# Kernel tuning notes

Measured on AMD Instinct MI355X. Metric: run time of the kernel, lower is better.

The kernel has to match this reference:

```python
import jax, jax.numpy as jnp
import numpy as np

SENS = 200
DM = 128
NMAPS = 2
NLAYERS = 2
TH = 0.01
EPS = 1e-5
BATCH = 8
SEQ = 96
HEADS = 8


def setup_inputs() -> dict:
    key = jax.random.key(0)
    ks = jax.random.split(key, 8)
    x = jax.random.normal(ks[0], (BATCH, SENS, SEQ, DM), jnp.float32)
    attn_s = jax.random.uniform(ks[1], (1, BATCH, HEADS, SENS, SENS), jnp.float32)
    supports = jax.random.uniform(ks[2], (SENS, SENS), jnp.float32)
    W_conv = jax.random.normal(ks[3], (NMAPS, NLAYERS, DM, DM), jnp.float32) * 0.05
    b_conv = jnp.zeros((NMAPS, NLAYERS, DM), jnp.float32)
    bn_gamma = jnp.ones((NMAPS, DM), jnp.float32)
    bn_beta = jnp.zeros((NMAPS, DM), jnp.float32)
    W_out = jax.random.normal(ks[4], (NMAPS * DM, DM), jnp.float32) * 0.05
    b_out = jnp.zeros((DM,), jnp.float32)
    return dict(x=x, attn_s=attn_s, supports=supports, W_conv=W_conv,
                b_conv=b_conv, bn_gamma=bn_gamma, bn_beta=bn_beta,
                W_out=W_out, b_out=b_out)


def _process_map(A):
    # make_symmetric: lower triangle + mirrored strict lower triangle
    A = jnp.tril(A) + jnp.tril(A, -1).T
    # clamp: threshold on absolute value; note original returns |A| thresholded
    Aa = jnp.abs(A)
    A = jnp.where(Aa > TH, Aa, jnp.zeros_like(Aa))
    # SparseTensor.from_dense(A).t()
    return A.T


def _gcn_norm(adj_t):
    # GCNConv default: add self-loops (weight 1), symmetric D^-1/2 A D^-1/2
    A = adj_t + jnp.eye(adj_t.shape[0], dtype=adj_t.dtype)
    deg = A.sum(axis=1)
    d = jnp.where(deg > 0, jax.lax.rsqrt(deg), jnp.zeros_like(deg))
    return d[:, None] * A * d[None, :]


def reference(x, attn_s, supports, W_conv, b_conv, bn_gamma, bn_beta, W_out, b_out):
    B, N, S, D = x.shape
    # reshape_mat: [B,N,S,D] -> [B*S, N, D]
    xr = x.transpose(0, 2, 1, 3).reshape(B * S, N, D)

    # supports: [data map, adaptive map from attention (mean over batch, heads)]
    maps = [_process_map(supports), _process_map(attn_s[0].mean(axis=(0, 1)))]

    gcn_outputs = []
    for i in range(NMAPS):
        An = _gcn_norm(maps[i])  # [N,N]
        h = jnp.zeros_like(xr[..., :1]) * 0.0  # placeholder replaced below
        h = None
        for l in range(NLAYERS):
            xw = jnp.einsum('bnf,fg->bng', xr, W_conv[i, l])
            hl = jnp.einsum('mn,bng->bmg', An, xw) + b_conv[i, l]
            h = hl if h is None else h + hl
        # BatchNorm1d over feature channel (training-mode batch stats, biased var)
        mu = h.mean(axis=(0, 1))
        var = h.var(axis=(0, 1))
        hn = (h - mu) * jax.lax.rsqrt(var + EPS) * bn_gamma[i] + bn_beta[i]
        gcn_outputs.append(jax.nn.relu(hn))

    cat = jnp.concatenate(gcn_outputs, axis=-1)  # [B*S, N, NMAPS*DM]
    y = jax.nn.relu(jnp.einsum('bnc,cd->bnd', cat, W_out) + b_out)
    # inverse_reshape_mat: [B*S, N, D] -> [B, N, S, D]
    return y.reshape(B, S, N, D).transpose(0, 2, 1, 3)
```

## Files before the change

kernel.cpp:

```cpp
#include <hip/hip_runtime.h>

#define SENS 200
#define DM 128
#define SEQ 96
#define NB 8
#define BS 768
#define NTOT 153600
#define TH 0.01f
#define BN_EPS 1e-5f
#define MPAD 224
#define KP 208
#define ASROW 68

typedef __attribute__((ext_vector_type(8)))  __bf16 bf16x8;
typedef __attribute__((ext_vector_type(4)))  __bf16 bf16x4;
typedef __attribute__((ext_vector_type(16))) float  f32x16;

__device__ __forceinline__ f32x16 mfma32(bf16x8 a, bf16x8 b, f32x16 c) {
    return __builtin_amdgcn_mfma_f32_32x32x16_bf16(a, b, c, 0, 0, 0);
}
__device__ __forceinline__ bf16x8 join8(bf16x4 a, bf16x4 b) {
    bf16x8 r;
    #pragma unroll
    for (int j = 0; j < 4; ++j) { r[j] = a[j]; r[j + 4] = b[j]; }
    return r;
}

__global__ void attn_mean_kernel(const float* __restrict__ attn, float* __restrict__ mapA) {
    int idx = blockIdx.x * 256 + threadIdx.x;
    if (idx >= SENS * SENS) return;
    float s = 0.f;
    #pragma unroll 8
    for (int q = 0; q < 64; ++q) s += attn[(size_t)q * SENS * SENS + idx];
    mapA[idx] = s * (1.0f / 64.0f);
}

__global__ void build_map_kernel(const float* __restrict__ supports, const float* __restrict__ mapA,
                                 float* __restrict__ M, float* __restrict__ deg) {
    __shared__ float red[256];
    int m = blockIdx.x, map = blockIdx.y, j = threadIdx.x;
    const float* src = (map == 0) ? supports : mapA;
    float v = 0.f;
    if (j < SENS) {
        float sym = (m >= j) ? src[m * SENS + j] : src[j * SENS + m];
        float a = fabsf(sym);
        v = (a > TH) ? a : 0.f;
        M[(size_t)map * SENS * SENS + m * SENS + j] = v;
    }
    red[j] = v;
    __syncthreads();
    for (int off = 128; off > 0; off >>= 1) {
        if (j < off) red[j] += red[j + off];
        __syncthreads();
    }
    if (j == 0) deg[map * SENS + m] = red[0] + 1.0f;
}

__global__ __launch_bounds__(256) void prep2_kernel(
    const float* __restrict__ M, const float* __restrict__ deg,
    const float* __restrict__ W_conv, const float* __restrict__ b_conv,
    const float* __restrict__ W_out,
    __bf16* __restrict__ Anb, __bf16* __restrict__ Wt, __bf16* __restrict__ Wot,
    float* __restrict__ bsum, float* __restrict__ bnacc)
{
    const int bid = blockIdx.x, t = threadIdx.x;
    if (bid < 2 * MPAD) {
        const int map = bid / MPAD, m = bid % MPAD;
        const int j = t;
        if (j < KP) {
            float val = 0.f;
            if (m < SENS && j < SENS) {
                float a = M[((size_t)map * SENS + m) * SENS + j] + ((m == j) ? 1.f : 0.f);
                val = rsqrtf(deg[map * SENS + m]) * a * rsqrtf(deg[map * SENS + j]);
            }
            Anb[(((size_t)map * 13 + (j >> 4)) * MPAD + m) * 16 + (j & 15)] = (__bf16)val;
        }
    } else {
        const int idx = (bid - 2 * MPAD) * 256 + t;
        if (idx < 32768) {
            const int map = idx >> 14, g = (idx >> 7) & 127, f = idx & 127;
            const float* wp = W_conv + (size_t)map * 2 * DM * DM + f * DM + g;
            Wt[(((size_t)map * 8 + (f >> 4)) * DM + g) * 16 + (f & 15)] = (__bf16)(wp[0] + wp[DM * DM]);
        } else if (idx < 65536) {
            const int k = idx - 32768, d = k >> 8, c = k & 255;
            Wot[(((size_t)(c >> 4)) * DM + d) * 16 + (c & 15)] = (__bf16)W_out[c * DM + d];
        } else if (idx < 65792) {
            const int k = idx - 65536, map = k >> 7, g = k & 127;
            bsum[k] = b_conv[(map * 2) * DM + g] + b_conv[(map * 2 + 1) * DM + g];
        } else if (idx < 66304) {
            bnacc[idx - 65792] = 0.f;
        }
    }
}

__global__ __launch_bounds__(256) void xprep_kernel(const float* __restrict__ x,
                                                    __bf16* __restrict__ xk) {
    const int n = blockIdx.x, b = blockIdx.y, t = threadIdx.x;
    const float* xp = x + ((size_t)b * SENS + n) * SEQ * DM;
    #pragma unroll 4
    for (int it = 0; it < 12; ++it) {
        const int idx = it * 1024 + t * 4;
        const int s = idx >> 7, f = idx & 127;
        float4 v = make_float4(0.f, 0.f, 0.f, 0.f);
        if (n < SENS) v = *(const float4*)(xp + idx);
        bf16x4 o;
        o[0] = (__bf16)v.x; o[1] = (__bf16)v.y; o[2] = (__bf16)v.z; o[3] = (__bf16)v.w;
        *(bf16x4*)(xk + (((size_t)(b * SEQ + s) * 8 + (f >> 4)) * MPAD + n) * 16 + (f & 15)) = o;
    }
}

__global__ __launch_bounds__(448, 6) void conv_kernel(
    const __bf16* __restrict__ xk, const __bf16* __restrict__ Anb,
    const __bf16* __restrict__ Wt, const float* __restrict__ bsum,
    __bf16* __restrict__ h, float* __restrict__ bnacc)
{
    __shared__ __bf16 xw[64 * KP];
    const int bx = blockIdx.x;
    const int bs = bx >> 2, map = (bx >> 1) & 1, gh = bx & 1;
    const int t = threadIdx.x, w = t >> 6, lane = t & 63;
    const int l31 = lane & 31, hi = lane >> 5;

    {
        f32x16 acc[2];
        #pragma unroll
        for (int p = 0; p < 2; ++p)
            #pragma unroll
            for (int r = 0; r < 16; ++r) acc[p][r] = 0.f;
        const __bf16* xb = xk + (((size_t)bs * 8) * MPAD + w * 32 + l31) * 16 + hi * 8;
        const __bf16* wb = Wt + (((size_t)map * 8) * DM + gh * 64 + l31) * 16 + hi * 8;
        #pragma unroll
        for (int kh = 0; kh < 2; ++kh) {
            bf16x8 bfr[4];
            #pragma unroll
            for (int q = 0; q < 4; ++q)
                bfr[q] = *(const bf16x8*)(xb + (size_t)(kh * 4 + q) * MPAD * 16);
            #pragma unroll
            for (int q = 0; q < 4; ++q) {
                const __bf16* wp = wb + (size_t)(kh * 4 + q) * DM * 16;
                acc[0] = mfma32(*(const bf16x8*)wp, bfr[q], acc[0]);
                acc[1] = mfma32(*(const bf16x8*)(wp + 32 * 16), bfr[q], acc[1]);
            }
        }
        const int n = w * 32 + l31;
        if (n < KP) {
            #pragma unroll
            for (int p = 0; p < 2; ++p)
                #pragma unroll
                for (int r = 0; r < 16; ++r) {
                    const int g = p * 32 + (r & 3) + 8 * (r >> 2) + 4 * hi;
                    xw[g * KP + n] = (__bf16)acc[p][r];
                }
        }
    }
    __syncthreads();

    f32x16 acc2[2];
    #pragma unroll
    for (int p = 0; p < 2; ++p)
        #pragma unroll
        for (int r = 0; r < 16; ++r) acc2[p][r] = 0.f;
    {
        const __bf16* ab = Anb + (((size_t)map * 13) * MPAD + w * 32 + l31) * 16 + hi * 8;
        #pragma unroll
        for (int kc = 0; kc < 13; ++kc) {
            bf16x8 afrag = *(const bf16x8*)(ab + (size_t)kc * MPAD * 16);
            #pragma unroll
            for (int p = 0; p < 2; ++p) {
                bf16x8 bfrag = *(const bf16x8*)(xw + (p * 32 + l31) * KP + kc * 16 + hi * 8);
                acc2[p] = mfma32(afrag, bfrag, acc2[p]);
            }
        }
    }
    float bsn[2], bsq[2];
    #pragma unroll
    for (int p = 0; p < 2; ++p) {
        const float bias = bsum[map * DM + gh * 64 + p * 32 + l31];
        bf16x8 h0, h1;
        float s = 0.f, q = 0.f;
        #pragma unroll
        for (int r = 0; r < 16; ++r) {
            const float v = acc2[p][r] + bias;
            if (r < 8) h0[r] = (__bf16)v; else h1[r - 8] = (__bf16)v;
            const int m = w * 32 + (r & 3) + 8 * (r >> 2) + 4 * hi;
            if (m < SENS) { s += v; q += v * v; }
        }
        __bf16* hp = h + ((((size_t)(bs * 2 + map) * 7 + w) * 4 + (gh * 2 + p)) * 64 + lane) * 16;
        *(bf16x8*)hp = h0;
        *(bf16x8*)(hp + 8) = h1;
        s += __shfl_xor(s, 32);
        q += __shfl_xor(q, 32);
        bsn[p] = s; bsq[p] = q;
    }
    __syncthreads();
    float* red = (float*)xw;
    if (hi == 0) {
        #pragma unroll
        for (int p = 0; p < 2; ++p) {
            red[(p * 32 + l31) * 7 + w] = bsn[p];
            red[(64 + p * 32 + l31) * 7 + w] = bsq[p];
        }
    }
    __syncthreads();
    if (t < 128) {
        const int sq = t >> 6, g = t & 63;
        float s = 0.f;
        #pragma unroll
        for (int k = 0; k < 7; ++k) s += red[(sq * 64 + g) * 7 + k];
        atomicAdd(&bnacc[sq * 256 + map * DM + gh * 64 + g], s);
    }
}

__device__ __forceinline__ void out_stage(int cn, int t, int bs,
                                          const __bf16* __restrict__ h,
                                          const float* sc_s, const float* sh_s,
                                          __bf16* dst)
{
    const int mapn = cn >> 1;
    const __bf16* hb = h + ((size_t)(bs * 2 + mapn) * 28 + (cn & 1) * 2) * 1024;
    bf16x8 vv[4];
    #pragma unroll
    for (int it = 0; it < 4; ++it) {
        const int idx = it * 512 + t;
        if (idx < 1792)
            vv[it] = *(const bf16x8*)(hb + ((size_t)(idx >> 8) * 4 + ((idx >> 7) & 1)) * 1024
                                          + ((idx >> 1) & 63) * 16 + (idx & 1) * 8);
    }
    #pragma unroll
    for (int it = 0; it < 4; ++it) {
        const int idx = it * 512 + t;
        if (idx < 1792) {
            const int half = idx & 1, lane_s = (idx >> 1) & 63;
            const int ctl = (idx >> 7) & 1, strip = idx >> 8;
            const int cl = ctl * 32 + (lane_s & 31);
            const int cg = mapn * DM + (cn & 1) * 64 + cl;
            const float scv = sc_s[cg], shv = sh_s[cg];
            const int mbase = strip * 32 + 4 * (lane_s >> 5) + 16 * half;
            #pragma unroll
            for (int q2 = 0; q2 < 8; ++q2) {
                const int row = mbase + (q2 & 3) + 8 * (q2 >> 2);
                const float fv = (float)vv[it][q2] * scv + shv;
                dst[row * ASROW + cl] = (__bf16)fmaxf(fv, 0.f);
            }
        }
    }
}

__global__ __launch_bounds__(512) void out_kernel(
    const __bf16* __restrict__ h, const __bf16* __restrict__ Wot,
    const float* __restrict__ bnacc,
    const float* __restrict__ gamma, const float* __restrict__ beta,
    const float* __restrict__ b_out, float* __restrict__ out)
{
    __shared__ __bf16 As[2][MPAD * ASROW];
    __shared__ float sc_s[256], sh_s[256];
    const int bs = blockIdx.x;
    const int b = bs / SEQ, s = bs % SEQ;
    const int t = threadIdx.x, w = t >> 6, lane = t & 63;
    const int l31 = lane & 31, hi = lane >> 5;
    const int dct = w & 3, sbase = w >> 2;
    if (t < 256) {
        const float mu = bnacc[t] * (1.f / (float)NTOT);
        const float var = bnacc[256 + t] * (1.f / (float)NTOT) - mu * mu;
        const float sc = gamma[t] * rsqrtf(var + BN_EPS);
        sc_s[t] = sc;
        sh_s[t] = beta[t] - mu * sc;
    }
    f32x16 acc[4];
    {
        const float bo = b_out[dct * 32 + l31];
        #pragma unroll
        for (int i = 0; i < 4; ++i)
            #pragma unroll
            for (int r = 0; r < 16; ++r) acc[i][r] = bo;
    }
    __syncthreads();
    out_stage(0, t, bs, h, sc_s, sh_s, &As[0][0]);
    __syncthreads();
    for (int c = 0; c < 4; ++c) {
        #pragma unroll
        for (int kc = 0; kc < 4; ++kc) {
            bf16x8 bfrag = *(const bf16x8*)(Wot + ((size_t)(c * 4 + kc) * DM + dct * 32 + l31) * 16 + hi * 8);
            #pragma unroll
            for (int i = 0; i < 4; ++i) {
                const int strip = sbase + 2 * i;
                if (strip >= 7) break;
                const __bf16* ap = &As[c & 1][(strip * 32 + l31) * ASROW + kc * 16 + hi * 8];
                acc[i] = mfma32(join8(*(const bf16x4*)ap, *(const bf16x4*)(ap + 4)), bfrag, acc[i]);
            }
        }
        if (c < 3) out_stage(c + 1, t, bs, h, sc_s, sh_s, &As[(c + 1) & 1][0]);
        __syncthreads();
    }
    #pragma unroll
    for (int i = 0; i < 4; ++i) {
        const int strip = sbase + 2 * i;
        if (strip >= 7) break;
        #pragma unroll
        for (int r = 0; r < 16; ++r) {
            const int m = strip * 32 + (r & 3) + 8 * (r >> 2) + 4 * hi;
            if (m < SENS)
                out[(((size_t)b * SENS + m) * SEQ + s) * DM + dct * 32 + l31] = fmaxf(acc[i][r], 0.f);
        }
    }
}

extern "C" void kernel_launch(void* const* d_in, const int* in_sizes, int n_in,
                              void* d_out, int out_size, void* d_ws, size_t ws_size,
                              hipStream_t stream) {
    const float* x        = (const float*)d_in[0];
    const float* attn     = (const float*)d_in[1];
    const float* supports = (const float*)d_in[2];
    const float* W_conv   = (const float*)d_in[3];
    const float* b_conv   = (const float*)d_in[4];
    const float* gamma    = (const float*)d_in[5];
    const float* beta     = (const float*)d_in[6];
    const float* W_out    = (const float*)d_in[7];
    const float* b_out    = (const float*)d_in[8];
    float* out = (float*)d_out;
    char* base = (char*)d_ws;

    float*  mapA  = (float*)(base + 0);
    float*  Mbuf  = (float*)(base + 160000);
    float*  deg   = (float*)(base + 480000);
    float*  bnacc = (float*)(base + 481664);
    float*  bsum  = (float*)(base + 483712);
    __bf16* Wt    = (__bf16*)(base + 484736);
    __bf16* Wot   = (__bf16*)(base + 550272);
    __bf16* Anb   = (__bf16*)(base + 615808);
    __bf16* xk    = (__bf16*)(base + 1048576);
    __bf16* h     = (__bf16*)(base + 45088768);

    attn_mean_kernel<<<157, 256, 0, stream>>>(attn, mapA);
    build_map_kernel<<<dim3(SENS, 2), 256, 0, stream>>>(supports, mapA, Mbuf, deg);
    prep2_kernel<<<2 * MPAD + 260, 256, 0, stream>>>(Mbuf, deg, W_conv, b_conv, W_out,
                                                     Anb, Wt, Wot, bsum, bnacc);
    xprep_kernel<<<dim3(MPAD, NB), 256, 0, stream>>>(x, xk);
    conv_kernel<<<BS * 4, 448, 0, stream>>>(xk, Anb, Wt, bsum, h, bnacc);
    out_kernel<<<BS, 512, 0, stream>>>(h, Wot, bnacc, gamma, beta, b_out, out);
}
```

Before: 289.6 us.

## Fuse x bf16 conversion into conv kernel and pad LDS row stride

Removes the separate xprep kernel and its bf16 staging buffer. The conv kernel now loads fp32 x rows directly and converts them to bf16 fragments in registers. This saves a launch and the intermediate write and read. The cost is that fp32 x is re-read by the four blocks sharing each (b,s), with strided rows. The LDS row stride is also padded from 208 to 212 to reduce bank conflicts on the xw tile.

New measurement: 274.4 us. 5.2% less time.

```diff
diff --git a/kernel.cpp b/kernel.cpp
--- a/kernel.cpp
+++ b/kernel.cpp
@@ -10,6 +10,7 @@
 #define BN_EPS 1e-5f
 #define MPAD 224
 #define KP 208
+#define XWS 212
 #define ASROW 68
 
 typedef __attribute__((ext_vector_type(8)))  __bf16 bf16x8;
@@ -93,30 +94,15 @@
     }
 }
 
-__global__ __launch_bounds__(256) void xprep_kernel(const float* __restrict__ x,
-                                                    __bf16* __restrict__ xk) {
-    const int n = blockIdx.x, b = blockIdx.y, t = threadIdx.x;
-    const float* xp = x + ((size_t)b * SENS + n) * SEQ * DM;
-    #pragma unroll 4
-    for (int it = 0; it < 12; ++it) {
-        const int idx = it * 1024 + t * 4;
-        const int s = idx >> 7, f = idx & 127;
-        float4 v = make_float4(0.f, 0.f, 0.f, 0.f);
-        if (n < SENS) v = *(const float4*)(xp + idx);
-        bf16x4 o;
-        o[0] = (__bf16)v.x; o[1] = (__bf16)v.y; o[2] = (__bf16)v.z; o[3] = (__bf16)v.w;
-        *(bf16x4*)(xk + (((size_t)(b * SEQ + s) * 8 + (f >> 4)) * MPAD + n) * 16 + (f & 15)) = o;
-    }
-}
-
 __global__ __launch_bounds__(448, 6) void conv_kernel(
-    const __bf16* __restrict__ xk, const __bf16* __restrict__ Anb,
+    const float* __restrict__ x, const __bf16* __restrict__ Anb,
     const __bf16* __restrict__ Wt, const float* __restrict__ bsum,
     __bf16* __restrict__ h, float* __restrict__ bnacc)
 {
-    __shared__ __bf16 xw[64 * KP];
+    __shared__ __bf16 xw[64 * XWS];
     const int bx = blockIdx.x;
     const int bs = bx >> 2, map = (bx >> 1) & 1, gh = bx & 1;
+    const int b = bs / SEQ, s = bs % SEQ;
     const int t = threadIdx.x, w = t >> 6, lane = t & 63;
     const int l31 = lane & 31, hi = lane >> 5;
 
@@ -126,29 +112,34 @@
         for (int p = 0; p < 2; ++p)
             #pragma unroll
             for (int r = 0; r < 16; ++r) acc[p][r] = 0.f;
-        const __bf16* xb = xk + (((size_t)bs * 8) * MPAD + w * 32 + l31) * 16 + hi * 8;
+        const int n = w * 32 + l31;
+        const bool valid = (n < SENS);
+        const float* xrow = x + (((size_t)b * SENS + (valid ? n : 0)) * SEQ + s) * DM + hi * 8;
         const __bf16* wb = Wt + (((size_t)map * 8) * DM + gh * 64 + l31) * 16 + hi * 8;
         #pragma unroll
-        for (int kh = 0; kh < 2; ++kh) {
-            bf16x8 bfr[4];
-            #pragma unroll
-            for (int q = 0; q < 4; ++q)
-                bfr[q] = *(const bf16x8*)(xb + (size_t)(kh * 4 + q) * MPAD * 16);
-            #pragma unroll
-            for (int q = 0; q < 4; ++q) {
-                const __bf16* wp = wb + (size_t)(kh * 4 + q) * DM * 16;
-                acc[0] = mfma32(*(const bf16x8*)wp, bfr[q], acc[0]);
-                acc[1] = mfma32(*(const bf16x8*)(wp + 32 * 16), bfr[q], acc[1]);
-            }
-        }
-        const int n = w * 32 + l31;
+        for (int kc = 0; kc < 8; ++kc) {
+            float4 v0 = *(const float4*)(xrow + kc * 16);
+            float4 v1 = *(const float4*)(xrow + kc * 16 + 4);
+            bf16x8 bfrag;
+            bfrag[0] = (__bf16)v0.x; bfrag[1] = (__bf16)v0.y;
+            bfrag[2] = (__bf16)v0.z; bfrag[3] = (__bf16)v0.w;
+            bfrag[4] = (__bf16)v1.x; bfrag[5] = (__bf16)v1.y;
+            bfrag[6] = (__bf16)v1.z; bfrag[7] = (__bf16)v1.w;
+            if (!valid) {
+                #pragma unroll
+                for (int j = 0; j < 8; ++j) bfrag[j] = (__bf16)0.f;
+            }
+            const __bf16* wp = wb + (size_t)kc * DM * 16;
+            acc[0] = mfma32(*(const bf16x8*)wp, bfrag, acc[0]);
+            acc[1] = mfma32(*(const bf16x8*)(wp + 32 * 16), bfrag, acc[1]);
+        }
         if (n < KP) {
             #pragma unroll
             for (int p = 0; p < 2; ++p)
                 #pragma unroll
                 for (int r = 0; r < 16; ++r) {
                     const int g = p * 32 + (r & 3) + 8 * (r >> 2) + 4 * hi;
-                    xw[g * KP + n] = (__bf16)acc[p][r];
+                    xw[g * XWS + n] = (__bf16)acc[p][r];
                 }
         }
     }
@@ -166,7 +157,7 @@
             bf16x8 afrag = *(const bf16x8*)(ab + (size_t)kc * MPAD * 16);
             #pragma unroll
             for (int p = 0; p < 2; ++p) {
-                bf16x8 bfrag = *(const bf16x8*)(xw + (p * 32 + l31) * KP + kc * 16 + hi * 8);
+                bf16x8 bfrag = *(const bf16x8*)(xw + (p * 32 + l31) * XWS + kc * 16 + hi * 8);
                 acc2[p] = mfma32(afrag, bfrag, acc2[p]);
             }
         }
@@ -176,20 +167,20 @@
     for (int p = 0; p < 2; ++p) {
         const float bias = bsum[map * DM + gh * 64 + p * 32 + l31];
         bf16x8 h0, h1;
-        float s = 0.f, q = 0.f;
+        float s2 = 0.f, q = 0.f;
         #pragma unroll
         for (int r = 0; r < 16; ++r) {
             const float v = acc2[p][r] + bias;
             if (r < 8) h0[r] = (__bf16)v; else h1[r - 8] = (__bf16)v;
             const int m = w * 32 + (r & 3) + 8 * (r >> 2) + 4 * hi;
-            if (m < SENS) { s += v; q += v * v; }
+            if (m < SENS) { s2 += v; q += v * v; }
         }
         __bf16* hp = h + ((((size_t)(bs * 2 + map) * 7 + w) * 4 + (gh * 2 + p)) * 64 + lane) * 16;
         *(bf16x8*)hp = h0;
         *(bf16x8*)(hp + 8) = h1;
-        s += __shfl_xor(s, 32);
+        s2 += __shfl_xor(s2, 32);
         q += __shfl_xor(q, 32);
-        bsn[p] = s; bsq[p] = q;
+        bsn[p] = s2; bsq[p] = q;
     }
     __syncthreads();
     float* red = (float*)xw;
@@ -203,10 +194,10 @@
     __syncthreads();
     if (t < 128) {
         const int sq = t >> 6, g = t & 63;
-        float s = 0.f;
-        #pragma unroll
-        for (int k = 0; k < 7; ++k) s += red[(sq * 64 + g) * 7 + k];
-        atomicAdd(&bnacc[sq * 256 + map * DM + gh * 64 + g], s);
+        float s2 = 0.f;
+        #pragma unroll
+        for (int k = 0; k < 7; ++k) s2 += red[(sq * 64 + g) * 7 + k];
+        atomicAdd(&bnacc[sq * 256 + map * DM + gh * 64 + g], s2);
     }
 }
 
@@ -327,14 +318,12 @@
     __bf16* Wt    = (__bf16*)(base + 484736);
     __bf16* Wot   = (__bf16*)(base + 550272);
     __bf16* Anb   = (__bf16*)(base + 615808);
-    __bf16* xk    = (__bf16*)(base + 1048576);
-    __bf16* h     = (__bf16*)(base + 45088768);
+    __bf16* h     = (__bf16*)(base + 1048576);
 
     attn_mean_kernel<<<157, 256, 0, stream>>>(attn, mapA);
     build_map_kernel<<<dim3(SENS, 2), 256, 0, stream>>>(supports, mapA, Mbuf, deg);
     prep2_kernel<<<2 * MPAD + 260, 256, 0, stream>>>(Mbuf, deg, W_conv, b_conv, W_out,
                                                      Anb, Wt, Wot, bsum, bnacc);
-    xprep_kernel<<<dim3(MPAD, NB), 256, 0, stream>>>(x, xk);
-    conv_kernel<<<BS * 4, 448, 0, stream>>>(xk, Anb, Wt, bsum, h, bnacc);
+    conv_kernel<<<BS * 4, 448, 0, stream>>>(x, Anb, Wt, bsum, h, bnacc);
     out_kernel<<<BS, 512, 0, stream>>>(h, Wot, bnacc, gamma, beta, b_out, out);
 }
```
